# Performance work log

Measured on AMD Instinct MI355X. Metric: run time of the kernel, lower is better.

The kernel has to match this reference:

```python
import jax, jax.numpy as jnp
import numpy as np

N = 50000      # nodes
E = 800000     # edges
DIN = 500      # input feature dim
H = 128        # hidden dim
C = 40         # num classes
B = 10000      # batch_size (labeled nodes)
L = 9          # n_layers
K = 5          # topk neighbors
ALPHA = 0.5
THETA = 1.0
ETA = 0.5


def setup_inputs() -> dict:
    key = jax.random.key(0)
    ks = jax.random.split(key, 10)
    x = jax.random.normal(ks[0], (N, DIN), jnp.float32)
    edge_index = jax.random.randint(ks[1], (2, E), 0, N, dtype=jnp.int32)
    edge_weight = jax.random.uniform(ks[2], (E,), jnp.float32)
    y = jax.random.randint(ks[3], (B,), 0, C, dtype=jnp.int32)
    W1 = jax.random.normal(ks[4], (DIN, H), jnp.float32) * 0.05
    b1 = jnp.zeros((H,), jnp.float32)
    conv_w1 = jax.random.normal(ks[5], (L, H, H), jnp.float32) * 0.05
    conv_w2 = jax.random.normal(ks[6], (L, H, H), jnp.float32) * 0.05
    W2 = jax.random.normal(ks[7], (H, C), jnp.float32) * 0.05
    b2 = jnp.zeros((C,), jnp.float32)
    return dict(x=x, edge_index=edge_index, edge_weight=edge_weight, y=y,
                batch_size=B, W1=W1, b1=b1, conv_w1=conv_w1, conv_w2=conv_w2,
                W2=W2, b2=b2)


def _spmm(edge_index, edge_weight, h):
    # out[row] += w * h[col]  (sparse adj_t @ h)
    row, col = edge_index[0], edge_index[1]
    msg = h[col] * edge_weight[:, None]           # [E, H]
    return jax.ops.segment_sum(msg, row, num_segments=N)


def reference(x, edge_index, edge_weight, y, batch_size, W1, b1, conv_w1, conv_w2, W2, b2):
    # eval mode: dropout is identity, no diagonal mask in label fusion
    h = jax.nn.relu(x @ W1 + b1)                  # [N, H]
    x0 = h
    for l in range(L):
        beta = float(np.log(THETA / (l + 1) + 1.0))
        p = _spmm(edge_index, edge_weight, h) * (1.0 - ALPHA)   # propagated, scaled
        xr = ALPHA * x0                                          # initial residual
        out = ((1.0 - beta) * p + beta * (p @ conv_w1[l])
               + (1.0 - beta) * xr + beta * (xr @ conv_w2[l]))
        h = jax.nn.relu(h + out)
    emb = h[:batch_size]                          # [B, H]
    logits = h @ W2 + b2
    p_lc = jax.nn.log_softmax(logits[:batch_size], axis=1)       # [B, C]
    # kNN label fusion: cosine similarity, topk, exp-weighted one-hot sum
    an = emb / jnp.clip(jnp.linalg.norm(emb, axis=1, keepdims=True), 1e-8)
    sim = an @ an.T                               # [B, B]
    vals, idx = jax.lax.top_k(sim, K)             # [B, K]
    w = jnp.exp(jax.lax.stop_gradient(vals))      # topk computed under no_grad
    onehot = jax.nn.one_hot(y, C, dtype=jnp.float32)             # [B, C]
    fused = jnp.einsum('bk,bkc->bc', w, onehot[idx])             # [B, C]
    p_sim = jax.nn.log_softmax(fused, axis=1)
    final = ETA * p_lc + (1.0 - ETA) * p_sim
    return final, emb
```

## Files before the change

### kernel.cpp

```cpp
#include <hip/hip_runtime.h>
#include <hip/hip_bf16.h>
#include <math.h>

#define Nn  50000
#define NR  50048
#define En  800000
#define DIN 500
#define Hd  128
#define Cc  40
#define Bb  10000
#define Ll  9
#define KT  5

typedef short bf16x8 __attribute__((ext_vector_type(8)));
typedef unsigned short u16x8 __attribute__((ext_vector_type(8)));
typedef float f32x4 __attribute__((ext_vector_type(4)));

__device__ inline float bf2f(unsigned short u) {
  union { unsigned int i; float f; } c; c.i = (unsigned int)u << 16; return c.f;
}
__device__ inline unsigned short f2bf(float f) {
  __hip_bfloat16 b = __float2bfloat16(f);
  return *(unsigned short*)&b;
}

__global__ __launch_bounds__(256) void k_pack_w1(const float* __restrict__ W1,
                                                 unsigned short* __restrict__ W1p) {
  const int id = blockIdx.x * 256 + threadIdx.x;
  if (id >= 65536) return;
  const int j = id & 7, col = (id >> 3) & 127, qk = id >> 10;
  const int k = (qk >> 2) * 32 + (qk & 3) * 8 + j;
  W1p[id] = f2bf((k < DIN) ? W1[(size_t)k * Hd + col] : 0.f);
}

__global__ __launch_bounds__(256) void k_pack_wc(const float* __restrict__ cw1,
    const float* __restrict__ cw2, unsigned short* __restrict__ Wcp) {
  const int id = blockIdx.x * 256 + threadIdx.x;
  if (id >= 294912) return;
  const int j = id & 7, col = (id >> 3) & 127, qk = (id >> 10) & 31, l = id >> 15;
  const int k = (qk >> 2) * 32 + (qk & 3) * 8 + j;
  float v;
  if (k < 128) v = cw1[((size_t)l * 128 + k) * 128 + col];
  else         v = 0.5f * cw2[((size_t)l * 128 + (k - 128)) * 128 + col];
  Wcp[id] = f2bf(v);
}

__global__ __launch_bounds__(256) void k_in(const float* __restrict__ x,
    const unsigned short* __restrict__ W1p, const float* __restrict__ b1,
    unsigned short* __restrict__ hb, unsigned short* __restrict__ x0b) {
  const int tid = threadIdx.x;
  const int wv = tid >> 6, lane = tid & 63;
  const int lrow = lane & 15, quad = lane >> 4;
  const int row0 = blockIdx.x * 64;
  const int ar = row0 + wv * 16 + lrow;
  f32x4 acc[8];
#pragma unroll
  for (int t = 0; t < 8; ++t) acc[t] = (f32x4){0.f, 0.f, 0.f, 0.f};

  for (int kk = 0; kk < 16; ++kk) {
    const int kbase = kk * 32 + quad * 8;
    float av[8];
    if (ar < Nn) {
      if (kk < 15) {
        const float4 p0 = *(const float4*)(x + (size_t)ar * DIN + kbase);
        const float4 p1 = *(const float4*)(x + (size_t)ar * DIN + kbase + 4);
        av[0] = p0.x; av[1] = p0.y; av[2] = p0.z; av[3] = p0.w;
        av[4] = p1.x; av[5] = p1.y; av[6] = p1.z; av[7] = p1.w;
      } else {
#pragma unroll
        for (int j = 0; j < 8; ++j)
          av[j] = (kbase + j < DIN) ? x[(size_t)ar * DIN + kbase + j] : 0.f;
      }
    } else {
#pragma unroll
      for (int j = 0; j < 8; ++j) av[j] = 0.f;
    }
    bf16x8 af;
#pragma unroll
    for (int j = 0; j < 8; ++j) af[j] = (short)f2bf(av[j]);
#pragma unroll
    for (int nt = 0; nt < 8; ++nt) {
      const bf16x8 bf = *(const bf16x8*)(W1p + ((size_t)(kk * 4 + quad) * 128 + nt * 16 + lrow) * 8);
      acc[nt] = __builtin_amdgcn_mfma_f32_16x16x32_bf16(af, bf, acc[nt], 0, 0, 0);
    }
  }

  __shared__ float sacc[64 * 132];
#pragma unroll
  for (int nt = 0; nt < 8; ++nt)
#pragma unroll
    for (int i = 0; i < 4; ++i)
      sacc[(wv * 16 + quad * 4 + i) * 132 + nt * 16 + lrow] = acc[nt][i];
  __syncthreads();

  const int row = tid >> 2, cs = (tid & 3) * 32;
  const int gr = row0 + row;
  if (gr < Nn) {
#pragma unroll
    for (int g = 0; g < 4; ++g) {
      const int c0 = cs + g * 8;
      float v[8];
#pragma unroll
      for (int j = 0; j < 8; ++j)
        v[j] = fmaxf(sacc[row * 132 + c0 + j] + b1[c0 + j], 0.f);
      u16x8 ob;
#pragma unroll
      for (int j = 0; j < 8; ++j) ob[j] = f2bf(v[j]);
      *(u16x8*)(hb + (size_t)gr * Hd + c0) = ob;
      *(u16x8*)(x0b + (size_t)gr * Hd + c0) = ob;
    }
  }
}

__global__ void k_hist(const int* __restrict__ rows, int* __restrict__ counts) {
  int e = blockIdx.x * 256 + threadIdx.x;
  if (e < En) atomicAdd(&counts[rows[e]], 1);
}

__global__ __launch_bounds__(256) void k_scan2(const int* __restrict__ counts,
                                               int* __restrict__ rptr) {
  __shared__ int sdata[256];
  const int b = blockIdx.x, tid = threadIdx.x;
  const int npre = b << 8;
  int s0 = 0, s1 = 0, s2 = 0, s3 = 0;
  int i = tid;
  for (; i + 768 < npre; i += 1024) {
    s0 += counts[i]; s1 += counts[i + 256]; s2 += counts[i + 512]; s3 += counts[i + 768];
  }
  for (; i < npre; i += 256) s0 += counts[i];
  sdata[tid] = s0 + s1 + s2 + s3;
  __syncthreads();
  for (int off = 128; off > 0; off >>= 1) {
    if (tid < off) sdata[tid] += sdata[tid + off];
    __syncthreads();
  }
  const int base = sdata[0];
  __syncthreads();
  const int gi = npre + tid;
  int v = (gi < Nn) ? counts[gi] : 0;
  sdata[tid] = v;
  __syncthreads();
  for (int off = 1; off < 256; off <<= 1) {
    int t = (tid >= off) ? sdata[tid - off] : 0;
    __syncthreads();
    sdata[tid] += t;
    __syncthreads();
  }
  if (gi < Nn) rptr[gi + 1] = base + sdata[tid];
  if (b == 0 && tid == 0) rptr[0] = 0;
}

__global__ void k_scatter(const int* __restrict__ rows, const int* __restrict__ cols,
                          const float* __restrict__ w, const int* __restrict__ ptr,
                          int* __restrict__ fill, int2* __restrict__ cpair) {
  int e = blockIdx.x * 256 + threadIdx.x;
  if (e >= En) return;
  int r = rows[e];
  int pos = atomicAdd(&fill[r], 1);
  int d = ptr[r] + pos;
  int2 pr; pr.x = cols[e]; pr.y = __float_as_int(w[e]);
  cpair[d] = pr;
}

__global__ __launch_bounds__(256) void k_spmm(const int* __restrict__ ptr,
    const int2* __restrict__ cpair,
    const unsigned short* __restrict__ hb, unsigned short* __restrict__ pb) {
  const int wave = (blockIdx.x * 256 + threadIdx.x) >> 6;
  const int lane = threadIdx.x & 63;
  const int g = lane >> 4;
  const int fl = lane & 15;
  if (wave >= Nn) return;
  const int s = ptr[wave], e_end = ptr[wave + 1];
  float acc[8];
#pragma unroll
  for (int j = 0; j < 8; ++j) acc[j] = 0.f;

  auto acc8 = [&](uint4 v, float w) {
    union { unsigned int i; float f; } t;
    t.i = v.x << 16;         acc[0] += w * t.f;
    t.i = v.x & 0xFFFF0000u; acc[1] += w * t.f;
    t.i = v.y << 16;         acc[2] += w * t.f;
    t.i = v.y & 0xFFFF0000u; acc[3] += w * t.f;
    t.i = v.z << 16;         acc[4] += w * t.f;
    t.i = v.z & 0xFFFF0000u; acc[5] += w * t.f;
    t.i = v.w << 16;         acc[6] += w * t.f;
    t.i = v.w & 0xFFFF0000u; acc[7] += w * t.f;
  };

  int e = s + g;
  for (; e + 12 < e_end; e += 16) {
    const int2 p0 = cpair[e];
    const int2 p1 = cpair[e + 4];
    const int2 p2 = cpair[e + 8];
    const int2 p3 = cpair[e + 12];
    const uint4 v0 = *(const uint4*)(hb + (size_t)p0.x * Hd + fl * 8);
    const uint4 v1 = *(const uint4*)(hb + (size_t)p1.x * Hd + fl * 8);
    const uint4 v2 = *(const uint4*)(hb + (size_t)p2.x * Hd + fl * 8);
    const uint4 v3 = *(const uint4*)(hb + (size_t)p3.x * Hd + fl * 8);
    acc8(v0, __int_as_float(p0.y)); acc8(v1, __int_as_float(p1.y));
    acc8(v2, __int_as_float(p2.y)); acc8(v3, __int_as_float(p3.y));
  }
  for (; e + 4 < e_end; e += 8) {
    const int2 p0 = cpair[e];
    const int2 p1 = cpair[e + 4];
    const uint4 v0 = *(const uint4*)(hb + (size_t)p0.x * Hd + fl * 8);
    const uint4 v1 = *(const uint4*)(hb + (size_t)p1.x * Hd + fl * 8);
    acc8(v0, __int_as_float(p0.y)); acc8(v1, __int_as_float(p1.y));
  }
  if (e < e_end) {
    const int2 p0 = cpair[e];
    const uint4 v = *(const uint4*)(hb + (size_t)p0.x * Hd + fl * 8);
    acc8(v, __int_as_float(p0.y));
  }
#pragma unroll
  for (int j = 0; j < 8; ++j) acc[j] += __shfl_xor(acc[j], 16);
#pragma unroll
  for (int j = 0; j < 8; ++j) acc[j] += __shfl_xor(acc[j], 32);
  if (g == 0) {
    uint4 o;
    o.x = (unsigned int)f2bf(0.5f * acc[0]) | ((unsigned int)f2bf(0.5f * acc[1]) << 16);
    o.y = (unsigned int)f2bf(0.5f * acc[2]) | ((unsigned int)f2bf(0.5f * acc[3]) << 16);
    o.z = (unsigned int)f2bf(0.5f * acc[4]) | ((unsigned int)f2bf(0.5f * acc[5]) << 16);
    o.w = (unsigned int)f2bf(0.5f * acc[6]) | ((unsigned int)f2bf(0.5f * acc[7]) << 16);
    *(uint4*)(pb + (size_t)wave * Hd + fl * 8) = o;
  }
}

__global__ __launch_bounds__(256) void k_layer(const unsigned short* __restrict__ pb,
    const unsigned short* __restrict__ x0b, const unsigned short* __restrict__ Wcp,
    unsigned short* __restrict__ hb, float beta) {
  const int tid = threadIdx.x;
  const int wv = tid >> 6, lane = tid & 63;
  const int lrow = lane & 15, quad = lane >> 4;
  const int row0 = blockIdx.x * 64;
  const int ar = row0 + wv * 16 + lrow;
  f32x4 acc[8];
#pragma unroll
  for (int t = 0; t < 8; ++t) acc[t] = (f32x4){0.f, 0.f, 0.f, 0.f};

#pragma unroll
  for (int kk = 0; kk < 8; ++kk) {
    const unsigned short* src = (kk < 4) ? pb : x0b;
    const int ko = (kk & 3) * 32 + quad * 8;
    const bf16x8 af = *(const bf16x8*)(src + (size_t)ar * Hd + ko);
#pragma unroll
    for (int nt = 0; nt < 8; ++nt) {
      const bf16x8 bf = *(const bf16x8*)(Wcp + ((size_t)(kk * 4 + quad) * 128 + nt * 16 + lrow) * 8);
      acc[nt] = __builtin_amdgcn_mfma_f32_16x16x32_bf16(af, bf, acc[nt], 0, 0, 0);
    }
  }

  __shared__ float sacc[64 * 132];
#pragma unroll
  for (int nt = 0; nt < 8; ++nt)
#pragma unroll
    for (int i = 0; i < 4; ++i)
      sacc[(wv * 16 + quad * 4 + i) * 132 + nt * 16 + lrow] = acc[nt][i];
  __syncthreads();

  const int row = tid >> 2, cs = (tid & 3) * 32;
  const int gr = row0 + row;
  if (gr < Nn) {
    const float om = 1.f - beta;
#pragma unroll
    for (int g = 0; g < 4; ++g) {
      const int c0 = cs + g * 8;
      const u16x8 pv = *(const u16x8*)(pb + (size_t)gr * Hd + c0);
      const u16x8 xv = *(const u16x8*)(x0b + (size_t)gr * Hd + c0);
      const u16x8 hv = *(const u16x8*)(hb + (size_t)gr * Hd + c0);
      float nv[8];
#pragma unroll
      for (int j = 0; j < 8; ++j) {
        const float gemm = sacc[row * 132 + c0 + j];
        const float pj = bf2f(pv[j]);
        const float xj = bf2f(xv[j]);
        const float outv = om * (pj + 0.5f * xj) + beta * gemm;
        nv[j] = fmaxf(bf2f(hv[j]) + outv, 0.f);
      }
      u16x8 ob;
#pragma unroll
      for (int j = 0; j < 8; ++j) ob[j] = f2bf(nv[j]);
      *(u16x8*)(hb + (size_t)gr * Hd + c0) = ob;
    }
  }
}

__global__ __launch_bounds__(256) void k_head(const unsigned short* __restrict__ hb,
    const float* __restrict__ W2, const float* __restrict__ b2,
    unsigned short* __restrict__ anb, float* __restrict__ p_lc,
    float* __restrict__ out_emb) {
  const int wid = (blockIdx.x * 256 + threadIdx.x) >> 6;
  const int lane = threadIdx.x & 63;
  if (wid >= Bb) return;
  const unsigned short* hr = hb + (size_t)wid * Hd;
  const float v0 = bf2f(hr[lane]), v1 = bf2f(hr[lane + 64]);
  out_emb[wid * Hd + lane] = v0;
  out_emb[wid * Hd + lane + 64] = v1;
  float ss = v0 * v0 + v1 * v1;
#pragma unroll
  for (int off = 32; off > 0; off >>= 1) ss += __shfl_xor(ss, off);
  const float inv = 1.f / fmaxf(sqrtf(ss), 1e-8f);
  anb[wid * Hd + lane] = f2bf(v0 * inv);
  anb[wid * Hd + lane + 64] = f2bf(v1 * inv);
  float l = 0.f;
  if (lane < Cc) {
    for (int k = 0; k < Hd; ++k) l += bf2f(hr[k]) * W2[k * Cc + lane];
    l += b2[lane];
  }
  float lm = (lane < Cc) ? l : -3.0e38f;
#pragma unroll
  for (int off = 32; off > 0; off >>= 1) lm = fmaxf(lm, __shfl_xor(lm, off));
  float ex = (lane < Cc) ? expf(l - lm) : 0.f;
#pragma unroll
  for (int off = 32; off > 0; off >>= 1) ex += __shfl_xor(ex, off);
  const float lse = logf(ex);
  if (lane < Cc) p_lc[wid * Cc + lane] = l - lm - lse;
}

#define CH_N  8
#define CH_SZ 1250
#define SB_LD 136
__global__ __launch_bounds__(256, 2) void k_simtopk(const unsigned short* __restrict__ anb,
    float* __restrict__ cval, int* __restrict__ cidx) {
  __shared__ __align__(16) unsigned short sb[64 * SB_LD];
  const int rt = blockIdx.x / CH_N;
  const int chunk = blockIdx.x % CH_N;
  const int row0 = rt * 64;
  const int cbeg = chunk * CH_SZ;
  const int cend = cbeg + CH_SZ;
  const int tid = threadIdx.x;
  const int wv = tid >> 6;
  const int lane = tid & 63;
  const int lrow = lane & 15;
  const int quad = lane >> 4;

  union Frag { uint4 u4; bf16x8 v; };
  bf16x8 afr[4];
  const int ar = row0 + wv * 16 + lrow;
#pragma unroll
  for (int kq = 0; kq < 4; ++kq) {
    Frag f;
    f.u4 = make_uint4(0u, 0u, 0u, 0u);
    if (ar < Bb) f.u4 = *(const uint4*)(anb + (size_t)ar * Hd + kq * 32 + quad * 8);
    afr[kq] = f.v;
  }

  float bv[4][KT];
  int bi[4][KT];
#pragma unroll
  for (int r = 0; r < 4; ++r)
#pragma unroll
    for (int t = 0; t < KT; ++t) { bv[r][t] = -3.0e38f; bi[r][t] = 0x7fffffff; }
  float minthr = -3.0e38f;

  const int ntile = (CH_SZ + 63) / 64;
  for (int t = 0; t < ntile; ++t) {
    const int c0 = cbeg + t * 64;
    __syncthreads();
    for (int i = tid; i < 1024; i += 256) {
      const int r = i >> 4, ch = i & 15;
      const int gc = c0 + r;
      uint4 v = make_uint4(0u, 0u, 0u, 0u);
      if (gc < cend) v = *(const uint4*)(anb + (size_t)gc * Hd + ch * 8);
      *(uint4*)&sb[r * SB_LD + ch * 8] = v;
    }
    __syncthreads();
#pragma unroll
    for (int sub = 0; sub < 4; ++sub) {
      f32x4 acc = {0.f, 0.f, 0.f, 0.f};
      const int scol = sub * 16 + lrow;
#pragma unroll
      for (int kq = 0; kq < 4; ++kq) {
        bf16x8 bfr = *(const bf16x8*)&sb[scol * SB_LD + kq * 32 + quad * 8];
        acc = __builtin_amdgcn_mfma_f32_16x16x32_bf16(afr[kq], bfr, acc, 0, 0, 0);
      }
      const int gc = c0 + scol;
      const bool ok = gc < cend;
      float vv[4];
#pragma unroll
      for (int i = 0; i < 4; ++i) vv[i] = ok ? acc[i] : -3.0e38f;
      const float mx = fmaxf(fmaxf(vv[0], vv[1]), fmaxf(vv[2], vv[3]));
      if (mx > minthr) {
#pragma unroll
        for (int i = 0; i < 4; ++i) {
          const float v = vv[i];
          if (v > bv[i][KT - 1]) {
            float tv = v; int ti = gc;
#pragma unroll
            for (int s = 0; s < KT; ++s) {
              if (tv > bv[i][s]) {
                float ov = bv[i][s]; int oi = bi[i][s];
                bv[i][s] = tv; bi[i][s] = ti; tv = ov; ti = oi;
              }
            }
          }
        }
        minthr = fminf(fminf(bv[0][KT - 1], bv[1][KT - 1]),
                       fminf(bv[2][KT - 1], bv[3][KT - 1]));
      }
    }
  }

#pragma unroll
  for (int off = 1; off < 16; off <<= 1) {
#pragma unroll
    for (int i = 0; i < 4; ++i) {
      float ov[KT]; int oi[KT];
#pragma unroll
      for (int t = 0; t < KT; ++t) {
        ov[t] = __shfl_xor(bv[i][t], off);
        oi[t] = __shfl_xor(bi[i][t], off);
      }
#pragma unroll
      for (int t = 0; t < KT; ++t) {
        float v = ov[t]; int id = oi[t];
        if (v > bv[i][KT - 1] || (v == bv[i][KT - 1] && id < bi[i][KT - 1])) {
#pragma unroll
          for (int s = 0; s < KT; ++s) {
            const bool take = (v > bv[i][s]) || (v == bv[i][s] && id < bi[i][s]);
            if (take) {
              float tv = bv[i][s]; int ti = bi[i][s];
              bv[i][s] = v; bi[i][s] = id; v = tv; id = ti;
            }
          }
        }
      }
    }
  }

  if (lrow == 0) {
#pragma unroll
    for (int i = 0; i < 4; ++i) {
      const int gr = row0 + wv * 16 + quad * 4 + i;
      if (gr < Bb) {
#pragma unroll
        for (int t = 0; t < KT; ++t) {
          cval[(size_t)gr * (CH_N * KT) + chunk * KT + t] = bv[i][t];
          cidx[(size_t)gr * (CH_N * KT) + chunk * KT + t] = bi[i][t];
        }
      }
    }
  }
}

__global__ __launch_bounds__(256) void k_final(const float* __restrict__ cval,
    const int* __restrict__ cidx, const int* __restrict__ y,
    const float* __restrict__ p_lc, float* __restrict__ out_final) {
  const int b = blockIdx.x * 256 + threadIdx.x;
  if (b >= Bb) return;
  float tv5[KT]; int ti5[KT];
#pragma unroll
  for (int t = 0; t < KT; ++t) { tv5[t] = -3.0e38f; ti5[t] = 0x7fffffff; }
  for (int m = 0; m < CH_N * KT; ++m) {
    float v = cval[(size_t)b * (CH_N * KT) + m]; int id = cidx[(size_t)b * (CH_N * KT) + m];
    if (v > tv5[KT - 1] || (v == tv5[KT - 1] && id < ti5[KT - 1])) {
#pragma unroll
      for (int t = 0; t < KT; ++t) {
        if (v > tv5[t] || (v == tv5[t] && id < ti5[t])) {
          float ov = tv5[t]; int oi = ti5[t];
          tv5[t] = v; ti5[t] = id; v = ov; id = oi;
        }
      }
    }
  }
  float w[KT]; int cls[KT];
#pragma unroll
  for (int t = 0; t < KT; ++t) { w[t] = expf(tv5[t]); cls[t] = y[ti5[t]]; }
  float m = -3.0e38f;
  for (int c = 0; c < Cc; ++c) {
    float f = 0.f;
#pragma unroll
    for (int t = 0; t < KT; ++t) f += (cls[t] == c) ? w[t] : 0.f;
    m = fmaxf(m, f);
  }
  float s = 0.f;
  for (int c = 0; c < Cc; ++c) {
    float f = 0.f;
#pragma unroll
    for (int t = 0; t < KT; ++t) f += (cls[t] == c) ? w[t] : 0.f;
    s += expf(f - m);
  }
  const float lse = logf(s);
  for (int c = 0; c < Cc; ++c) {
    float f = 0.f;
#pragma unroll
    for (int t = 0; t < KT; ++t) f += (cls[t] == c) ? w[t] : 0.f;
    out_final[b * Cc + c] = 0.5f * p_lc[b * Cc + c] + 0.5f * (f - m - lse);
  }
}

extern "C" void kernel_launch(void* const* d_in, const int* in_sizes, int n_in,
                              void* d_out, int out_size, void* d_ws, size_t ws_size,
                              hipStream_t stream) {
  const float* x  = (const float*)d_in[0];
  const int* erow = (const int*)d_in[1];
  const int* ecol = erow + En;
  const float* ew = (const float*)d_in[2];
  const int* y    = (const int*)d_in[3];
  const float* W1 = (const float*)d_in[5];
  const float* b1 = (const float*)d_in[6];
  const float* cw1 = (const float*)d_in[7];
  const float* cw2 = (const float*)d_in[8];
  const float* W2 = (const float*)d_in[9];
  const float* b2 = (const float*)d_in[10];
  float* out = (float*)d_out;

  float* ws = (float*)d_ws;
  size_t off = 0;
  float* plc = ws + off; off += (size_t)Bb * Cc;
  float* cval = ws + off; off += (size_t)Bb * (CH_N * KT);
  int* cidx  = (int*)(ws + off); off += (size_t)Bb * (CH_N * KT);
  int* counts = (int*)(ws + off); off += Nn;
  int* fill   = (int*)(ws + off); off += Nn;
  int* rptr   = (int*)(ws + off); off += Nn + 4;
  int2* cpair = (int2*)(ws + off); off += (size_t)2 * En;
  unsigned short* anb = (unsigned short*)(ws + off); off += (size_t)Bb * Hd / 2;
  unsigned short* hb  = (unsigned short*)(ws + off); off += (size_t)NR * Hd / 2;
  unsigned short* x0b = (unsigned short*)(ws + off); off += (size_t)NR * Hd / 2;
  unsigned short* pb  = (unsigned short*)(ws + off); off += (size_t)NR * Hd / 2;
  unsigned short* W1p = (unsigned short*)(ws + off); off += 65536 / 2;
  unsigned short* Wcp = (unsigned short*)(ws + off); off += 294912 / 2;

  k_pack_w1<<<256, 256, 0, stream>>>(W1, W1p);
  k_pack_wc<<<1152, 256, 0, stream>>>(cw1, cw2, Wcp);
  k_in<<<NR / 64, 256, 0, stream>>>(x, W1p, b1, hb, x0b);
  hipMemsetAsync(counts, 0, (size_t)2 * Nn * sizeof(int), stream);
  k_hist<<<(En + 255) / 256, 256, 0, stream>>>(erow, counts);
  k_scan2<<<(Nn + 255) / 256, 256, 0, stream>>>(counts, rptr);
  k_scatter<<<(En + 255) / 256, 256, 0, stream>>>(erow, ecol, ew, rptr, fill, cpair);
  for (int l = 0; l < Ll; ++l) {
    const float beta = logf(1.0f / (float)(l + 1) + 1.0f);
    k_spmm<<<(Nn * 64 + 255) / 256, 256, 0, stream>>>(rptr, cpair, hb, pb);
    k_layer<<<NR / 64, 256, 0, stream>>>(pb, x0b, Wcp + (size_t)l * 32768, hb, beta);
  }
  k_head<<<(Bb * 64) / 256, 256, 0, stream>>>(hb, W2, b2, anb, plc, out + (size_t)Bb * Cc);
  k_simtopk<<<((Bb + 63) / 64) * CH_N, 256, 0, stream>>>(anb, cval, cidx);
  k_final<<<(Bb + 255) / 256, 256, 0, stream>>>(cval, cidx, y, plc, out);
}
```

Measured before the change: 992.9 us.

## Fuse SpMM aggregation with per-layer GEMM using LDS and ping-pong h buffers

Merges the per-layer sparse aggregation kernel and the dense layer kernel into one. Each block gathers its 64 rows into LDS, then runs the MFMA GEMM and epilogue from LDS, so the propagated features never round-trip through global memory. Because a layer can no longer update h in place while other blocks gather from it, h now alternates between two buffers. The cost is less parallelism in the gather: each wave walks 16 rows in sequence instead of one wave per row, and LDS use per block goes up, which may reduce occupancy and latency hiding.

```diff
diff --git a/kernel.cpp b/kernel.cpp
--- a/kernel.cpp
+++ b/kernel.cpp
@@ -162,100 +162,105 @@
   cpair[d] = pr;
 }
 
-__global__ __launch_bounds__(256) void k_spmm(const int* __restrict__ ptr,
-    const int2* __restrict__ cpair,
-    const unsigned short* __restrict__ hb, unsigned short* __restrict__ pb) {
-  const int wave = (blockIdx.x * 256 + threadIdx.x) >> 6;
-  const int lane = threadIdx.x & 63;
+#define PB_LD 136
+__global__ __launch_bounds__(256) void k_fused(const int* __restrict__ ptr,
+    const int2* __restrict__ cpair, const unsigned short* __restrict__ hbr,
+    const unsigned short* __restrict__ x0b, const unsigned short* __restrict__ Wcp,
+    unsigned short* __restrict__ hbw, float beta) {
+  __shared__ __align__(16) unsigned short pb_s[64 * PB_LD];
+  __shared__ float sacc[64 * 132];
+  const int tid = threadIdx.x;
+  const int wv = tid >> 6, lane = tid & 63;
   const int g = lane >> 4;
   const int fl = lane & 15;
-  if (wave >= Nn) return;
-  const int s = ptr[wave], e_end = ptr[wave + 1];
-  float acc[8];
-#pragma unroll
-  for (int j = 0; j < 8; ++j) acc[j] = 0.f;
-
-  auto acc8 = [&](uint4 v, float w) {
-    union { unsigned int i; float f; } t;
-    t.i = v.x << 16;         acc[0] += w * t.f;
-    t.i = v.x & 0xFFFF0000u; acc[1] += w * t.f;
-    t.i = v.y << 16;         acc[2] += w * t.f;
-    t.i = v.y & 0xFFFF0000u; acc[3] += w * t.f;
-    t.i = v.z << 16;         acc[4] += w * t.f;
-    t.i = v.z & 0xFFFF0000u; acc[5] += w * t.f;
-    t.i = v.w << 16;         acc[6] += w * t.f;
-    t.i = v.w & 0xFFFF0000u; acc[7] += w * t.f;
-  };
-
-  int e = s + g;
-  for (; e + 12 < e_end; e += 16) {
-    const int2 p0 = cpair[e];
-    const int2 p1 = cpair[e + 4];
-    const int2 p2 = cpair[e + 8];
-    const int2 p3 = cpair[e + 12];
-    const uint4 v0 = *(const uint4*)(hb + (size_t)p0.x * Hd + fl * 8);
-    const uint4 v1 = *(const uint4*)(hb + (size_t)p1.x * Hd + fl * 8);
-    const uint4 v2 = *(const uint4*)(hb + (size_t)p2.x * Hd + fl * 8);
-    const uint4 v3 = *(const uint4*)(hb + (size_t)p3.x * Hd + fl * 8);
-    acc8(v0, __int_as_float(p0.y)); acc8(v1, __int_as_float(p1.y));
-    acc8(v2, __int_as_float(p2.y)); acc8(v3, __int_as_float(p3.y));
-  }
-  for (; e + 4 < e_end; e += 8) {
-    const int2 p0 = cpair[e];
-    const int2 p1 = cpair[e + 4];
-    const uint4 v0 = *(const uint4*)(hb + (size_t)p0.x * Hd + fl * 8);
-    const uint4 v1 = *(const uint4*)(hb + (size_t)p1.x * Hd + fl * 8);
-    acc8(v0, __int_as_float(p0.y)); acc8(v1, __int_as_float(p1.y));
-  }
-  if (e < e_end) {
-    const int2 p0 = cpair[e];
-    const uint4 v = *(const uint4*)(hb + (size_t)p0.x * Hd + fl * 8);
-    acc8(v, __int_as_float(p0.y));
-  }
-#pragma unroll
-  for (int j = 0; j < 8; ++j) acc[j] += __shfl_xor(acc[j], 16);
-#pragma unroll
-  for (int j = 0; j < 8; ++j) acc[j] += __shfl_xor(acc[j], 32);
-  if (g == 0) {
-    uint4 o;
-    o.x = (unsigned int)f2bf(0.5f * acc[0]) | ((unsigned int)f2bf(0.5f * acc[1]) << 16);
-    o.y = (unsigned int)f2bf(0.5f * acc[2]) | ((unsigned int)f2bf(0.5f * acc[3]) << 16);
-    o.z = (unsigned int)f2bf(0.5f * acc[4]) | ((unsigned int)f2bf(0.5f * acc[5]) << 16);
-    o.w = (unsigned int)f2bf(0.5f * acc[6]) | ((unsigned int)f2bf(0.5f * acc[7]) << 16);
-    *(uint4*)(pb + (size_t)wave * Hd + fl * 8) = o;
-  }
-}
-
-__global__ __launch_bounds__(256) void k_layer(const unsigned short* __restrict__ pb,
-    const unsigned short* __restrict__ x0b, const unsigned short* __restrict__ Wcp,
-    unsigned short* __restrict__ hb, float beta) {
-  const int tid = threadIdx.x;
-  const int wv = tid >> 6, lane = tid & 63;
+  const int row0 = blockIdx.x * 64;
+
+  for (int r = 0; r < 16; ++r) {
+    const int row = row0 + wv * 16 + r;
+    float acc[8];
+#pragma unroll
+    for (int j = 0; j < 8; ++j) acc[j] = 0.f;
+
+    auto acc8 = [&](uint4 v, float w) {
+      union { unsigned int i; float f; } t;
+      t.i = v.x << 16;         acc[0] += w * t.f;
+      t.i = v.x & 0xFFFF0000u; acc[1] += w * t.f;
+      t.i = v.y << 16;         acc[2] += w * t.f;
+      t.i = v.y & 0xFFFF0000u; acc[3] += w * t.f;
+      t.i = v.z << 16;         acc[4] += w * t.f;
+      t.i = v.z & 0xFFFF0000u; acc[5] += w * t.f;
+      t.i = v.w << 16;         acc[6] += w * t.f;
+      t.i = v.w & 0xFFFF0000u; acc[7] += w * t.f;
+    };
+
+    if (row < Nn) {
+      const int s = ptr[row], e_end = ptr[row + 1];
+      int e = s + g;
+      for (; e + 12 < e_end; e += 16) {
+        const int2 p0 = cpair[e];
+        const int2 p1 = cpair[e + 4];
+        const int2 p2 = cpair[e + 8];
+        const int2 p3 = cpair[e + 12];
+        const uint4 v0 = *(const uint4*)(hbr + (size_t)p0.x * Hd + fl * 8);
+        const uint4 v1 = *(const uint4*)(hbr + (size_t)p1.x * Hd + fl * 8);
+        const uint4 v2 = *(const uint4*)(hbr + (size_t)p2.x * Hd + fl * 8);
+        const uint4 v3 = *(const uint4*)(hbr + (size_t)p3.x * Hd + fl * 8);
+        acc8(v0, __int_as_float(p0.y)); acc8(v1, __int_as_float(p1.y));
+        acc8(v2, __int_as_float(p2.y)); acc8(v3, __int_as_float(p3.y));
+      }
+      for (; e + 4 < e_end; e += 8) {
+        const int2 p0 = cpair[e];
+        const int2 p1 = cpair[e + 4];
+        const uint4 v0 = *(const uint4*)(hbr + (size_t)p0.x * Hd + fl * 8);
+        const uint4 v1 = *(const uint4*)(hbr + (size_t)p1.x * Hd + fl * 8);
+        acc8(v0, __int_as_float(p0.y)); acc8(v1, __int_as_float(p1.y));
+      }
+      if (e < e_end) {
+        const int2 p0 = cpair[e];
+        const uint4 v = *(const uint4*)(hbr + (size_t)p0.x * Hd + fl * 8);
+        acc8(v, __int_as_float(p0.y));
+      }
+    }
+#pragma unroll
+    for (int j = 0; j < 8; ++j) acc[j] += __shfl_xor(acc[j], 16);
+#pragma unroll
+    for (int j = 0; j < 8; ++j) acc[j] += __shfl_xor(acc[j], 32);
+    if (g == 0) {
+      uint4 o;
+      o.x = (unsigned int)f2bf(0.5f * acc[0]) | ((unsigned int)f2bf(0.5f * acc[1]) << 16);
+      o.y = (unsigned int)f2bf(0.5f * acc[2]) | ((unsigned int)f2bf(0.5f * acc[3]) << 16);
+      o.z = (unsigned int)f2bf(0.5f * acc[4]) | ((unsigned int)f2bf(0.5f * acc[5]) << 16);
+      o.w = (unsigned int)f2bf(0.5f * acc[6]) | ((unsigned int)f2bf(0.5f * acc[7]) << 16);
+      *(uint4*)&pb_s[(wv * 16 + r) * PB_LD + fl * 8] = o;
+    }
+  }
+  __syncthreads();
+
   const int lrow = lane & 15, quad = lane >> 4;
-  const int row0 = blockIdx.x * 64;
   const int ar = row0 + wv * 16 + lrow;
-  f32x4 acc[8];
-#pragma unroll
-  for (int t = 0; t < 8; ++t) acc[t] = (f32x4){0.f, 0.f, 0.f, 0.f};
+  const int arl = wv * 16 + lrow;
+  f32x4 gacc[8];
+#pragma unroll
+  for (int t = 0; t < 8; ++t) gacc[t] = (f32x4){0.f, 0.f, 0.f, 0.f};
 
 #pragma unroll
   for (int kk = 0; kk < 8; ++kk) {
-    const unsigned short* src = (kk < 4) ? pb : x0b;
     const int ko = (kk & 3) * 32 + quad * 8;
-    const bf16x8 af = *(const bf16x8*)(src + (size_t)ar * Hd + ko);
+    bf16x8 af;
+    if (kk < 4) af = *(const bf16x8*)&pb_s[arl * PB_LD + ko];
+    else        af = *(const bf16x8*)(x0b + (size_t)ar * Hd + ko);
 #pragma unroll
     for (int nt = 0; nt < 8; ++nt) {
       const bf16x8 bf = *(const bf16x8*)(Wcp + ((size_t)(kk * 4 + quad) * 128 + nt * 16 + lrow) * 8);
-      acc[nt] = __builtin_amdgcn_mfma_f32_16x16x32_bf16(af, bf, acc[nt], 0, 0, 0);
-    }
-  }
-
-  __shared__ float sacc[64 * 132];
+      gacc[nt] = __builtin_amdgcn_mfma_f32_16x16x32_bf16(af, bf, gacc[nt], 0, 0, 0);
+    }
+  }
+
 #pragma unroll
   for (int nt = 0; nt < 8; ++nt)
 #pragma unroll
     for (int i = 0; i < 4; ++i)
-      sacc[(wv * 16 + quad * 4 + i) * 132 + nt * 16 + lrow] = acc[nt][i];
+      sacc[(wv * 16 + quad * 4 + i) * 132 + nt * 16 + lrow] = gacc[nt][i];
   __syncthreads();
 
   const int row = tid >> 2, cs = (tid & 3) * 32;
@@ -263,11 +268,11 @@
   if (gr < Nn) {
     const float om = 1.f - beta;
 #pragma unroll
-    for (int g = 0; g < 4; ++g) {
-      const int c0 = cs + g * 8;
-      const u16x8 pv = *(const u16x8*)(pb + (size_t)gr * Hd + c0);
+    for (int gg = 0; gg < 4; ++gg) {
+      const int c0 = cs + gg * 8;
+      const u16x8 pv = *(const u16x8*)&pb_s[row * PB_LD + c0];
       const u16x8 xv = *(const u16x8*)(x0b + (size_t)gr * Hd + c0);
-      const u16x8 hv = *(const u16x8*)(hb + (size_t)gr * Hd + c0);
+      const u16x8 hv = *(const u16x8*)(hbr + (size_t)gr * Hd + c0);
       float nv[8];
 #pragma unroll
       for (int j = 0; j < 8; ++j) {
@@ -280,7 +285,7 @@
       u16x8 ob;
 #pragma unroll
       for (int j = 0; j < 8; ++j) ob[j] = f2bf(nv[j]);
-      *(u16x8*)(hb + (size_t)gr * Hd + c0) = ob;
+      *(u16x8*)(hbw + (size_t)gr * Hd + c0) = ob;
     }
   }
 }
@@ -515,25 +520,28 @@
   int* rptr   = (int*)(ws + off); off += Nn + 4;
   int2* cpair = (int2*)(ws + off); off += (size_t)2 * En;
   unsigned short* anb = (unsigned short*)(ws + off); off += (size_t)Bb * Hd / 2;
-  unsigned short* hb  = (unsigned short*)(ws + off); off += (size_t)NR * Hd / 2;
+  unsigned short* hba = (unsigned short*)(ws + off); off += (size_t)NR * Hd / 2;
+  unsigned short* hbb = (unsigned short*)(ws + off); off += (size_t)NR * Hd / 2;
   unsigned short* x0b = (unsigned short*)(ws + off); off += (size_t)NR * Hd / 2;
-  unsigned short* pb  = (unsigned short*)(ws + off); off += (size_t)NR * Hd / 2;
   unsigned short* W1p = (unsigned short*)(ws + off); off += 65536 / 2;
   unsigned short* Wcp = (unsigned short*)(ws + off); off += 294912 / 2;
 
   k_pack_w1<<<256, 256, 0, stream>>>(W1, W1p);
   k_pack_wc<<<1152, 256, 0, stream>>>(cw1, cw2, Wcp);
-  k_in<<<NR / 64, 256, 0, stream>>>(x, W1p, b1, hb, x0b);
+  k_in<<<NR / 64, 256, 0, stream>>>(x, W1p, b1, hba, x0b);
   hipMemsetAsync(counts, 0, (size_t)2 * Nn * sizeof(int), stream);
   k_hist<<<(En + 255) / 256, 256, 0, stream>>>(erow, counts);
   k_scan2<<<(Nn + 255) / 256, 256, 0, stream>>>(counts, rptr);
   k_scatter<<<(En + 255) / 256, 256, 0, stream>>>(erow, ecol, ew, rptr, fill, cpair);
+  unsigned short* hcur = hba;
+  unsigned short* hnxt = hbb;
   for (int l = 0; l < Ll; ++l) {
     const float beta = logf(1.0f / (float)(l + 1) + 1.0f);
-    k_spmm<<<(Nn * 64 + 255) / 256, 256, 0, stream>>>(rptr, cpair, hb, pb);
-    k_layer<<<NR / 64, 256, 0, stream>>>(pb, x0b, Wcp + (size_t)l * 32768, hb, beta);
-  }
-  k_head<<<(Bb * 64) / 256, 256, 0, stream>>>(hb, W2, b2, anb, plc, out + (size_t)Bb * Cc);
+    k_fused<<<NR / 64, 256, 0, stream>>>(rptr, cpair, hcur, x0b,
+                                         Wcp + (size_t)l * 32768, hnxt, beta);
+    unsigned short* t = hcur; hcur = hnxt; hnxt = t;
+  }
+  k_head<<<(Bb * 64) / 256, 256, 0, stream>>>(hcur, W2, b2, anb, plc, out + (size_t)Bb * Cc);
   k_simtopk<<<((Bb + 63) / 64) * CH_N, 256, 0, stream>>>(anb, cval, cidx);
   k_final<<<(Bb + 255) / 256, 256, 0, stream>>>(cval, cidx, y, plc, out);
 }
```

After: 1.253 ms. +26.2%, slower.
